# Performance work log

Hardware: AMD Instinct MI355X
Metric: run time of the kernel (lower is better)

The kernel has to match this reference:

```python
import jax, jax.numpy as jnp
import numpy as np

B, NB, D, T, K = 8, 3, 512, 2048, 1024


def setup_inputs() -> dict:
    key = jax.random.key(0)
    k1, k2 = jax.random.split(key)
    x = jax.random.normal(k1, (B, NB, D, T), dtype=jnp.float32)
    codebook = jax.random.normal(k2, (NB, K, D), dtype=jnp.float32)
    return {"x": x, "codebook": codebook}


def reference(x, codebook):
    """Band vector quantization forward.

    x:        [B, NB, D, T]  (channels-first frames, one chunk per band)
    codebook: [NB, K, D]     (one Euclidean codebook per band)
    Returns (quantized [B,NB,D,T], codes [B,NB,T] int32, commit_loss scalar).
    """
    xt = jnp.swapaxes(x, -1, -2)  # [B, NB, T, D]
    x2 = jnp.sum(xt * xt, axis=-1, keepdims=True)          # [B, NB, T, 1]
    e2 = jnp.sum(codebook * codebook, axis=-1)              # [NB, K]
    xe = jnp.einsum('bntd,nkd->bntk', xt, codebook)         # [B, NB, T, K]
    dist = x2 - 2.0 * xe + e2[None, :, None, :]
    codes = jnp.argmin(dist, axis=-1)                       # [B, NB, T]
    # gather nearest codewords per band
    band_idx = jnp.arange(NB).reshape(1, NB, 1)
    q = codebook[band_idx, codes]                           # [B, NB, T, D]
    # commitment loss: MSE(sg(quantized), x), mean over bands
    commit_loss = jnp.mean((jax.lax.stop_gradient(q) - xt) ** 2)
    # straight-through estimator
    q_st = xt + jax.lax.stop_gradient(q - xt)
    quantized = jnp.swapaxes(q_st, -1, -2)                  # [B, NB, D, T]
    return quantized, codes, commit_loss
```

## Files before the change

kernel.cpp:

```cpp
#include <hip/hip_runtime.h>


#define B_ 8
#define NB_ 3
#define D_ 512
#define T_ 2048
#define K_ 1024
#define BN_ (B_*NB_)
#define ROWS_ (BN_*T_)
#define Q_ELEMS_ ((size_t)BN_*D_*T_)
#define MARGIN_ 0.10f
#define WINDOW_ 0.30f
#define FLAGCAP_ 8192
#define RESCAN_BLOCKS_ 2048
#define QSCALE_ (1.0f / (float)Q_ELEMS_)

typedef __attribute__((ext_vector_type(4))) float f32x4;
typedef __attribute__((ext_vector_type(8))) _Float16 f16x8;
typedef __attribute__((ext_vector_type(4))) unsigned int u32x4;

__device__ inline unsigned short f2h(float f) {
    _Float16 h = (_Float16)f;
    return __builtin_bit_cast(unsigned short, h);
}
__device__ inline void gld16(const void* g, void* l) {
    __builtin_amdgcn_global_load_lds(
        (const __attribute__((address_space(1))) unsigned int*)g,
        (__attribute__((address_space(3))) unsigned int*)l, 16, 0, 0);
}

__global__ __launch_bounds__(256) void convert_all(
    const float* __restrict__ x, const float* __restrict__ cb,
    unsigned short* __restrict__ Xh, unsigned short* __restrict__ Eh,
    float* __restrict__ e2, float* __restrict__ lossp,
    int* __restrict__ flag_cnt) {
    int tid = threadIdx.x;
    if (blockIdx.y == 8) {
        int bid = blockIdx.x + 32 * blockIdx.z;
        if (bid == 0 && tid == 0) { *lossp = 0.f; *flag_cnt = 0; }
        int row = bid * 4 + (tid >> 6);
        int lane = tid & 63;
        const float* p = cb + (size_t)row * D_ + lane * 8;
        float v[8];
#pragma unroll
        for (int e = 0; e < 8; ++e) v[e] = p[e];
        double sum = 0.0;
#pragma unroll
        for (int e = 0; e < 8; ++e) sum += (double)v[e] * (double)v[e];
        unsigned int uh[4];
#pragma unroll
        for (int q = 0; q < 4; ++q)
            uh[q] = (unsigned)f2h(v[2*q]) | ((unsigned)f2h(v[2*q+1]) << 16);
        *(u32x4*)((char*)Eh + (size_t)row * 1024 + lane * 16) =
            u32x4{uh[0], uh[1], uh[2], uh[3]};
        for (int off = 32; off > 0; off >>= 1) sum += __shfl_down(sum, off, 64);
        if (lane == 0) e2[row] = (float)sum;
        return;
    }
    int t0 = blockIdx.x * 64;
    int sl = blockIdx.y;
    int bn = blockIdx.z;
    int d0 = sl * 64;
    __shared__ float tile[64][69];
    int tt4 = (tid & 15) * 4, ddl = tid >> 4;
#pragma unroll
    for (int p = 0; p < 4; ++p) {
        int dd = ddl + 16 * p;
        float4 v = *(const float4*)&x[((size_t)bn * D_ + d0 + dd) * T_ + t0 + tt4];
        tile[dd][tt4 + 0] = v.x; tile[dd][tt4 + 1] = v.y;
        tile[dd][tt4 + 2] = v.z; tile[dd][tt4 + 3] = v.w;
    }
    __syncthreads();
    int tt = tid >> 2, cp = tid & 3;
    size_t rowbyte = ((size_t)bn * T_ + t0 + tt) * 1024 + (size_t)sl * 128;
    float s2 = 0.f;
#pragma unroll
    for (int cc = 0; cc < 2; ++cc) {
        int c = cp + 4 * cc;
        unsigned int uh[4];
#pragma unroll
        for (int q = 0; q < 4; ++q) {
            float v0 = tile[c * 8 + 2*q][tt], v1 = tile[c * 8 + 2*q + 1][tt];
            s2 += v0 * v0 + v1 * v1;
            uh[q] = (unsigned)f2h(v0) | ((unsigned)f2h(v1) << 16);
        }
        *(u32x4*)((char*)Xh + rowbyte + c * 16) = u32x4{uh[0], uh[1], uh[2], uh[3]};
    }
    for (int off = 32; off > 0; off >>= 1) s2 += __shfl_down(s2, off, 64);
    __shared__ float ws4[4];
    if ((tid & 63) == 0) ws4[tid >> 6] = s2;
    __syncthreads();
    if (tid == 0)
        atomicAdd(lossp, (ws4[0] + ws4[1] + ws4[2] + ws4[3]) * QSCALE_);
}

__global__ __launch_bounds__(256, 4) void vq_gemm(
    const unsigned short* __restrict__ Xh, const unsigned short* __restrict__ Eh,
    const float* __restrict__ e2,
    float* __restrict__ pm1, float* __restrict__ pm2, int* __restrict__ pi1) {

    __shared__ char lds[32768];
    int tid = threadIdx.x;
    int lane = tid & 63, wid = tid >> 6;
    int bx = blockIdx.x, by = blockIdx.y, bn = blockIdx.z;
    int band = bn % NB_;
    int wm = wid >> 1, wn = wid & 1;
    int rl = lane & 15, cl = lane >> 4;

    int is_b = wid >> 1;
    int wq = wid & 1;
    const char* srcm = is_b ? (const char*)Eh : (const char*)Xh;
    size_t rowbase = is_b ? ((size_t)band * K_ + (size_t)by * 128)
                          : ((size_t)bn * T_ + (size_t)bx * 128);
    const char* lane_src = srcm + (rowbase + wq * 64 + (lane >> 2)) * 1024
                         + (((lane & 3) ^ ((lane >> 3) & 3)) * 16);
    const int dstoff = is_b * 8192 + wq * 4096;
    const int chunkoff = ((cl ^ ((rl >> 1) & 3)) * 16);

    int kb = by * 128 + wn * 64 + rl;
    float ev[4];
#pragma unroll
    for (int n = 0; n < 4; ++n) ev[n] = e2[band * K_ + kb + n * 16];

    f32x4 acc[4][4];
#pragma unroll
    for (int m = 0; m < 4; ++m)
#pragma unroll
        for (int n = 0; n < 4; ++n) acc[m][n] = f32x4{0.f, 0.f, 0.f, 0.f};

    {
        char* dp = lds + dstoff;
#pragma unroll
        for (int q = 0; q < 4; ++q) gld16(lane_src + (size_t)q * 16384, dp + q * 1024);
    }

    for (int s = 0; s < 16; ++s) {
        asm volatile("s_waitcnt vmcnt(0)" ::: "memory");
        __builtin_amdgcn_s_barrier();

        if (s < 15) {
            const char* sp = lane_src + (size_t)(s + 1) * 64;
            char* dp = lds + ((s + 1) & 1) * 16384 + dstoff;
#pragma unroll
            for (int q = 0; q < 4; ++q) gld16(sp + (size_t)q * 16384, dp + q * 1024);
        }

        const char* base = lds + (s & 1) * 16384;
        f16x8 bh[4];
#pragma unroll
        for (int n = 0; n < 4; ++n)
            bh[n] = *(const f16x8*)(base + 8192 + (wn * 64 + n * 16 + rl) * 64 + chunkoff);
#pragma unroll
        for (int m = 0; m < 4; ++m) {
            f16x8 ah = *(const f16x8*)(base + (wm * 64 + m * 16 + rl) * 64 + chunkoff);
#pragma unroll
            for (int n = 0; n < 4; ++n)
                acc[m][n] = __builtin_amdgcn_mfma_f32_16x16x32_f16(ah, bh[n], acc[m][n], 0, 0, 0);
        }
    }

    float tm1[16], tm2[16];
    int ti[16];
#pragma unroll
    for (int m = 0; m < 4; ++m)
#pragma unroll
        for (int r = 0; r < 4; ++r) {
            int id = m * 4 + r;
            float a1 = 3.4e38f, a2 = 3.4e38f; int i1 = 0;
#pragma unroll
            for (int n = 0; n < 4; ++n) {
                float v = fmaf(-2.0f, acc[m][n][r], ev[n]);
                int k = kb + n * 16;
                a2 = fminf(fmaxf(v, a1), a2);
                if (v < a1) { a1 = v; i1 = k; }
            }
            tm1[id] = a1; tm2[id] = a2; ti[id] = i1;
        }
#pragma unroll
    for (int id = 0; id < 16; ++id) {
#pragma unroll
        for (int st = 1; st < 16; st <<= 1) {
            float om1 = __shfl_xor(tm1[id], st, 64);
            float om2 = __shfl_xor(tm2[id], st, 64);
            int   oi  = __shfl_xor(ti[id],  st, 64);
            if (om1 < tm1[id] || (om1 == tm1[id] && oi < ti[id])) {
                tm2[id] = fminf(tm1[id], om2); tm1[id] = om1; ti[id] = oi;
            } else {
                tm2[id] = fminf(tm2[id], om1);
            }
        }
    }
    float* mm1 = (float*)lds;
    float* mm2 = (float*)(lds + 1024);
    int*   mi  = (int*)(lds + 2048);
    __syncthreads();
    if (rl == 0) {
#pragma unroll
        for (int m = 0; m < 4; ++m)
#pragma unroll
            for (int r = 0; r < 4; ++r) {
                int row = wm * 64 + m * 16 + cl * 4 + r;
                mm1[wn * 128 + row] = tm1[m * 4 + r];
                mm2[wn * 128 + row] = tm2[m * 4 + r];
                mi [wn * 128 + row] = ti [m * 4 + r];
            }
    }
    __syncthreads();
    if (tid < 128) {
        float m1 = mm1[tid], m2 = mm2[tid]; int i1 = mi[tid];
        float b1 = mm1[128 + tid], b2 = mm2[128 + tid]; int bi = mi[128 + tid];
        if (b1 < m1 || (b1 == m1 && bi < i1)) { m2 = fminf(m1, b2); m1 = b1; i1 = bi; }
        else m2 = fminf(m2, b1);
        size_t gr = (size_t)bn * T_ + (size_t)bx * 128 + tid;
        pm1[gr * 8 + by] = m1; pm2[gr * 8 + by] = m2; pi1[gr * 8 + by] = i1;
    }
}

__global__ __launch_bounds__(256) void finalize_kernel(
    const float* __restrict__ pm1, const float* __restrict__ pm2,
    const int* __restrict__ pi1,
    float* __restrict__ outc, float* __restrict__ lossp,
    int* __restrict__ flag_cnt, int* __restrict__ flag_list) {
    int row = blockIdx.x * 256 + threadIdx.x;
    size_t r8 = (size_t)row * 8;
    float m1 = pm1[r8], m2 = pm2[r8]; int i1 = pi1[r8];
#pragma unroll
    for (int j = 1; j < 8; ++j) {
        float b1 = pm1[r8 + j], b2 = pm2[r8 + j]; int bi = pi1[r8 + j];
        if (b1 < m1) { m2 = fminf(m1, b2); m1 = b1; i1 = bi; }
        else m2 = fminf(m2, b1);
    }
    float lrow = m1;
    if (m2 - m1 < MARGIN_) {
        int slot = atomicAdd(flag_cnt, 1);
        if (slot < FLAGCAP_) { flag_list[slot] = row; lrow = 0.f; }
        else outc[row] = (float)i1;
    } else {
        outc[row] = (float)i1;
    }
    for (int off = 32; off > 0; off >>= 1) lrow += __shfl_down(lrow, off, 64);
    __shared__ float ws4[4];
    if ((threadIdx.x & 63) == 0) ws4[threadIdx.x >> 6] = lrow;
    __syncthreads();
    if (threadIdx.x == 0)
        atomicAdd(lossp, (ws4[0] + ws4[1] + ws4[2] + ws4[3]) * QSCALE_);
}

__global__ __launch_bounds__(256) void rescan_kernel(
    const float* __restrict__ x, const float* __restrict__ cb,
    const float* __restrict__ pm1,
    const int* __restrict__ flag_cnt, const int* __restrict__ flag_list,
    float* __restrict__ outc, float* __restrict__ lossp) {
    int tid = threadIdx.x;
    int cnt = *flag_cnt; if (cnt > FLAGCAP_) cnt = FLAGCAP_;
    __shared__ float xsh[D_];
    __shared__ float qm[8];
    __shared__ double rv[256];
    __shared__ int    ri[256];
    for (int i = blockIdx.x; i < cnt; i += RESCAN_BLOCKS_) {
        int row = flag_list[i];
        int bn = row / T_, t = row % T_;
        int band = bn % NB_;
        __syncthreads();
        if (tid < 8) qm[tid] = pm1[(size_t)row * 8 + tid];
        for (int d = tid; d < D_; d += 256)
            xsh[d] = x[((size_t)bn * D_ + d) * T_ + t];
        __syncthreads();
        float gmin = qm[0];
#pragma unroll
        for (int j = 1; j < 8; ++j) gmin = fminf(gmin, qm[j]);
        double px2 = 0.0;
        for (int d = tid; d < D_; d += 256) px2 += (double)xsh[d] * (double)xsh[d];
        rv[tid] = px2;
        __syncthreads();
        for (int s2 = 128; s2 > 0; s2 >>= 1) {
            if (tid < s2) rv[tid] += rv[tid + s2];
            __syncthreads();
        }
        double x2row = rv[0];
        __syncthreads();

        int kq = tid >> 1, half = tid & 1;
        double best = 1e300; int bi = K_;
        for (int j = 0; j < 8; ++j) {
            if (qm[j] > gmin + WINDOW_) continue;
            int k = j * 128 + kq;
            const float* cr = cb + ((size_t)band * K_ + k) * D_ + half * 256;
            const float* xr = xsh + half * 256;
            double s = 0.0;
#pragma unroll 4
            for (int d = 0; d < 256; d += 4) {
                float4 c4 = *(const float4*)(cr + d);
                double e0 = (double)xr[d]     - (double)c4.x;
                double e1 = (double)xr[d + 1] - (double)c4.y;
                double e2v = (double)xr[d + 2] - (double)c4.z;
                double e3 = (double)xr[d + 3] - (double)c4.w;
                s += e0 * e0 + e1 * e1 + e2v * e2v + e3 * e3;
            }
            s += __shfl_xor(s, 1, 64);
            if (s < best || (s == best && k < bi)) { best = s; bi = k; }
        }
        rv[tid] = best; ri[tid] = bi;
        __syncthreads();
        for (int s2 = 128; s2 > 0; s2 >>= 1) {
            if (tid < s2) {
                if (rv[tid + s2] < rv[tid] ||
                    (rv[tid + s2] == rv[tid] && ri[tid + s2] < ri[tid])) {
                    rv[tid] = rv[tid + s2]; ri[tid] = ri[tid + s2];
                }
            }
            __syncthreads();
        }
        if (tid == 0) {
            outc[row] = (float)ri[0];
            atomicAdd(lossp, (float)((rv[0] - x2row) * (double)QSCALE_));
        }
        __syncthreads();
    }
}

__global__ __launch_bounds__(256) void gather_out(
    const float* __restrict__ cb, const float* __restrict__ outc,
    float* __restrict__ outq) {
    int t0 = blockIdx.x * 256;
    int d0 = blockIdx.y * 16;
    int bn = blockIdx.z;
    int band = bn % NB_;
    int tid = threadIdx.x;
    __shared__ int csh[256];
    __shared__ float qsh[16][260];
    csh[tid] = (int)outc[(size_t)bn * T_ + t0 + tid];
    __syncthreads();
    const float* cbb = cb + (size_t)band * K_ * D_ + d0;
    int tq = tid >> 2, dq = (tid & 3) * 4;
#pragma unroll
    for (int p = 0; p < 4; ++p) {
        int t = tq + p * 64;
        float4 v = *(const float4*)(cbb + (size_t)csh[t] * D_ + dq);
        qsh[dq + 0][t] = v.x; qsh[dq + 1][t] = v.y;
        qsh[dq + 2][t] = v.z; qsh[dq + 3][t] = v.w;
    }
    __syncthreads();
    int wv = tid >> 6, ln = tid & 63;
#pragma unroll
    for (int j = 0; j < 4; ++j) {
        int dd = wv * 4 + j;
        *(float4*)&outq[((size_t)bn * D_ + d0 + dd) * T_ + t0 + ln * 4] =
            *(const float4*)&qsh[dd][ln * 4];
    }
}

extern "C" void kernel_launch(void* const* d_in, const int* in_sizes, int n_in,
                              void* d_out, int out_size, void* d_ws, size_t ws_size,
                              hipStream_t stream) {
    (void)in_sizes; (void)n_in; (void)out_size; (void)ws_size;
    const float* x  = (const float*)d_in[0];
    const float* cb = (const float*)d_in[1];
    float* out = (float*)d_out;

    float* outq  = out;
    float* outc  = out + Q_ELEMS_;
    float* lossp = out + Q_ELEMS_ + ROWS_;

    unsigned short* Xh = (unsigned short*)d_out;
    float* pm1 = out + 13107200;
    float* pm2 = pm1 + (size_t)ROWS_ * 8;
    int*   pi1 = (int*)(pm2 + (size_t)ROWS_ * 8);

    char* ws = (char*)d_ws;
    unsigned short* Eh = (unsigned short*)ws;
    float* e2  = (float*)(Eh + (size_t)NB_ * K_ * D_);
    int*   flag_cnt  = (int*)(e2 + NB_ * K_);
    int*   flag_list = flag_cnt + 1;

    convert_all<<<dim3(32, 9, 24), dim3(256), 0, stream>>>(
        x, cb, Xh, Eh, e2, lossp, flag_cnt);
    vq_gemm<<<dim3(16, 8, 24), dim3(256), 0, stream>>>(Xh, Eh, e2, pm1, pm2, pi1);
    finalize_kernel<<<dim3(ROWS_ / 256), dim3(256), 0, stream>>>(
        pm1, pm2, pi1, outc, lossp, flag_cnt, flag_list);
    rescan_kernel<<<dim3(RESCAN_BLOCKS_), dim3(256), 0, stream>>>(
        x, cb, pm1, flag_cnt, flag_list, outc, lossp);
    gather_out<<<dim3(8, 32, 24), dim3(256), 0, stream>>>(cb, outc, outq);
}
```

Baseline: 254.6 us.

## Replace direct global-to-LDS loads with register-staged double-buffered prefetch

The GEMM tile loop stops using global_load_lds and instead loads each tile into registers two stages ahead, writing it to the alternate LDS buffer while the current buffer feeds the MFMAs. The vmcnt(0) wait at the top of each iteration is replaced by an lgkmcnt wait and barrier at the end, so global latency can overlap with compute over more than one stage. It costs extra VGPRs for the staging registers and explicit LDS store instructions, which may reduce occupancy.

```diff
diff --git a/kernel.cpp b/kernel.cpp
--- a/kernel.cpp
+++ b/kernel.cpp
@@ -23,11 +23,6 @@
     _Float16 h = (_Float16)f;
     return __builtin_bit_cast(unsigned short, h);
 }
-__device__ inline void gld16(const void* g, void* l) {
-    __builtin_amdgcn_global_load_lds(
-        (const __attribute__((address_space(1))) unsigned int*)g,
-        (__attribute__((address_space(3))) unsigned int*)l, 16, 0, 0);
-}
 
 __global__ __launch_bounds__(256) void convert_all(
     const float* __restrict__ x, const float* __restrict__ cb,
@@ -114,7 +109,7 @@
                           : ((size_t)bn * T_ + (size_t)bx * 128);
     const char* lane_src = srcm + (rowbase + wq * 64 + (lane >> 2)) * 1024
                          + (((lane & 3) ^ ((lane >> 3) & 3)) * 16);
-    const int dstoff = is_b * 8192 + wq * 4096;
+    const int lds_woff = is_b * 8192 + wq * 4096 + lane * 16;
     const int chunkoff = ((cl ^ ((rl >> 1) & 3)) * 16);
 
     int kb = by * 128 + wn * 64 + rl;
@@ -128,23 +123,34 @@
 #pragma unroll
         for (int n = 0; n < 4; ++n) acc[m][n] = f32x4{0.f, 0.f, 0.f, 0.f};
 
-    {
-        char* dp = lds + dstoff;
-#pragma unroll
-        for (int q = 0; q < 4; ++q) gld16(lane_src + (size_t)q * 16384, dp + q * 1024);
-    }
+    u32x4 r[4];
+
+#define LOADT_(t)                                                          \
+    {                                                                      \
+        const char* sp_ = lane_src + (size_t)(t) * 64;                     \
+        _Pragma("unroll")                                                  \
+        for (int q = 0; q < 4; ++q)                                        \
+            r[q] = *(const u32x4*)(sp_ + (size_t)q * 16384);               \
+    }
+#define WRITET_(buf)                                                       \
+    {                                                                      \
+        char* wb_ = lds + (buf) * 16384 + lds_woff;                        \
+        _Pragma("unroll")                                                  \
+        for (int q = 0; q < 4; ++q)                                        \
+            *(u32x4*)(wb_ + q * 1024) = r[q];                              \
+    }
+
+    LOADT_(0);
+    WRITET_(0);
+    LOADT_(1);
+    asm volatile("s_waitcnt lgkmcnt(0)" ::: "memory");
+    __builtin_amdgcn_s_barrier();
 
     for (int s = 0; s < 16; ++s) {
-        asm volatile("s_waitcnt vmcnt(0)" ::: "memory");
-        __builtin_amdgcn_s_barrier();
-
         if (s < 15) {
-            const char* sp = lane_src + (size_t)(s + 1) * 64;
-            char* dp = lds + ((s + 1) & 1) * 16384 + dstoff;
-#pragma unroll
-            for (int q = 0; q < 4; ++q) gld16(sp + (size_t)q * 16384, dp + q * 1024);
-        }
-
+            WRITET_((s + 1) & 1);
+            if (s < 14) LOADT_(s + 2);
+        }
         const char* base = lds + (s & 1) * 16384;
         f16x8 bh[4];
 #pragma unroll
@@ -157,19 +163,23 @@
             for (int n = 0; n < 4; ++n)
                 acc[m][n] = __builtin_amdgcn_mfma_f32_16x16x32_f16(ah, bh[n], acc[m][n], 0, 0, 0);
         }
-    }
+        asm volatile("s_waitcnt lgkmcnt(0)" ::: "memory");
+        __builtin_amdgcn_s_barrier();
+    }
+#undef LOADT_
+#undef WRITET_
 
     float tm1[16], tm2[16];
     int ti[16];
 #pragma unroll
     for (int m = 0; m < 4; ++m)
 #pragma unroll
-        for (int r = 0; r < 4; ++r) {
-            int id = m * 4 + r;
+        for (int rr = 0; rr < 4; ++rr) {
+            int id = m * 4 + rr;
             float a1 = 3.4e38f, a2 = 3.4e38f; int i1 = 0;
 #pragma unroll
             for (int n = 0; n < 4; ++n) {
-                float v = fmaf(-2.0f, acc[m][n][r], ev[n]);
+                float v = fmaf(-2.0f, acc[m][n][rr], ev[n]);
                 int k = kb + n * 16;
                 a2 = fminf(fmaxf(v, a1), a2);
                 if (v < a1) { a1 = v; i1 = k; }
@@ -198,11 +208,11 @@
 #pragma unroll
         for (int m = 0; m < 4; ++m)
 #pragma unroll
-            for (int r = 0; r < 4; ++r) {
-                int row = wm * 64 + m * 16 + cl * 4 + r;
-                mm1[wn * 128 + row] = tm1[m * 4 + r];
-                mm2[wn * 128 + row] = tm2[m * 4 + r];
-                mi [wn * 128 + row] = ti [m * 4 + r];
+            for (int rr = 0; rr < 4; ++rr) {
+                int row = wm * 64 + m * 16 + cl * 4 + rr;
+                mm1[wn * 128 + row] = tm1[m * 4 + rr];
+                mm2[wn * 128 + row] = tm2[m * 4 + rr];
+                mi [wn * 128 + row] = ti [m * 4 + rr];
             }
     }
     __syncthreads();
```

Result: no change. 253.3 us (-0.5%).
